# Kernel tuning notes

Measured on AMD Instinct MI355X. Metric: run time of the kernel, lower is better.

## Reference

```python
import jax, jax.numpy as jnp
import numpy as np
from jax import lax

EPS = 1e-5

def _bn(x):
    # BatchNorm1d, training-mode batch stats, affine at init (gamma=1, beta=0)
    return (x - x.mean(0)) / jnp.sqrt(x.var(0) + EPS)

def _nonlinear(x, W1, W2):
    h = jax.nn.relu(_bn(x @ W1.T))
    return jax.nn.relu(_bn(h @ W2.T))

def _conv_bn_lrelu(x, w):
    # x: [E, C, L], w: [O, C, 3], padding=1; BN over (batch, length)
    y = lax.conv_general_dilated(x, w, (1,), [(1, 1)], dimension_numbers=('NCH', 'OIH', 'NCH'))
    m = y.mean((0, 2), keepdims=True)
    v = y.var((0, 2), keepdims=True)
    y = (y - m) / jnp.sqrt(v + EPS)
    return jnp.where(y >= 0, y, 0.01 * y)  # LeakyReLU(negative_slope=0.01)

def _curve_encoder(x, c1, c2, c3, fc):
    y = _conv_bn_lrelu(x, c1)
    y = _conv_bn_lrelu(y, c2)
    y = _conv_bn_lrelu(y, c3)
    y = y.mean(-1)            # AdaptiveAvgPool1d(1)
    return _bn(y @ fc.T)      # _fc: Linear(bias=False) + BN, no activation

def _forward(attn_bias, angle, centroid_distance, edge_data, edge_type,
             edge_length, edge_convexity, node_feat,
             sd_emb, virt, angle_W1, angle_W2, cent_W1, cent_W2,
             etype_W1, etype_W2, elen_W1, elen_W2, econv_W1, econv_W2,
             curv_c1, curv_c2, curv_c3, curv_fc, edis_w,
             ec_Wp, ec_W1, ec_W2,
             shortest_distance, edge_path, edge_padding_mask, src, dst):
    B, N, _ = shortest_distance.shape
    H = sd_emb.shape[1]
    D = edge_path.shape[-1]           # multi_hop_max_dist
    n_edge = edge_padding_mask.shape[1]

    bias = jnp.broadcast_to(attn_bias[:, None], (B, H, N + 1, N + 1))

    # shortest-distance / angle / centroid biases, all [B, H, N, N]
    sdb = sd_emb[shortest_distance].transpose(0, 3, 1, 2)
    ang = _nonlinear(angle.reshape(-1, 1), angle_W1, angle_W2).reshape(B, N, N, H).transpose(0, 3, 1, 2)
    cen = _nonlinear(centroid_distance.reshape(-1, 1), cent_W1, cent_W2).reshape(B, N, N, H).transpose(0, 3, 1, 2)

    # --- multi_hop branch ---
    ef = (_curve_encoder(edge_data.transpose(0, 2, 1), curv_c1, curv_c2, curv_c3, curv_fc)
          + _nonlinear(edge_type, etype_W1, etype_W2)
          + _nonlinear(edge_length[:, None], elen_W1, elen_W2)
          + _nonlinear(edge_convexity, econv_W1, econv_W2))     # [E, H]
    # EdgeConv (UV-Net style node_cat): proj(n[src]) + proj(n[dst]) + efeat -> MLP -> BN -> ReLU
    proj = node_feat @ ec_Wp.T
    agg = proj[src] + proj[dst] + ef
    h = jax.nn.relu(_bn(agg @ ec_W1.T)) @ ec_W2.T
    ef2 = jax.nn.relu(_bn(h))                                   # [E, H]

    # edge_padding_mask is all-False, so edge_feature[edge_pos] = ef2 is a plain
    # row-major reshape; slot n_edge stays zero (padding target of edge_path)
    edge_feature = jnp.zeros((B, n_edge + 1, H), dtype=edge_data.dtype)
    edge_feature = edge_feature.at[:, :n_edge].set(ef2.reshape(B, n_edge, H))

    sd_ = jnp.where(shortest_distance == 0, 1, shortest_distance)
    sd_ = jnp.where(sd_ > 1, sd_ - 1, sd_)
    sd_ = jnp.clip(sd_, 0, D)

    ep = edge_path.reshape(B, N * N * D)
    eb = jnp.take_along_axis(edge_feature, ep[:, :, None], axis=1).reshape(B, N, N, D, H)
    Wd = edis_w.reshape(-1, H, H)[:D]                           # [D, H, H]
    eb = jnp.einsum('bijdh,dhk->bijk', eb, Wd)                  # per-hop bmm fused with hop-sum
    eb = eb / (sd_.astype(eb.dtype)[..., None] + 1e-6)
    eb = jnp.nan_to_num(eb)
    ebias = eb.transpose(0, 3, 1, 2)                            # [B, H, N, N]

    bias = bias.at[:, :, 1:, 1:].add(sdb + ang + cen + ebias)
    t = virt.reshape(1, H, 1)
    bias = bias.at[:, :, 1:, 0].add(t)
    bias = bias.at[:, :, 0, :].add(t)
    return bias + attn_bias[:, None]


def setup_inputs() -> dict:
    key = jax.random.key(0)
    ks = iter(jax.random.split(key, 48))
    B, N, H, D = 4, 256, 16, 5
    n_edge, n_pts = 1024, 20
    dim_node, num_distance, num_edge_dis = 256, 512, 128
    E = B * n_edge
    tot_nodes = B * N
    rn = lambda *s: jax.random.normal(next(ks), s, jnp.float32)
    return {
        'attn_bias': rn(B, N + 1, N + 1),
        'shortest_distance': jax.random.randint(next(ks), (B, N, N), 0, num_distance),
        'angle': rn(B, N, N),
        'centroid_distance': rn(B, N, N),
        'edge_path': jax.random.randint(next(ks), (B, N, N, D), 0, n_edge + 1),
        'edge_data': rn(E, n_pts, 12),
        'edge_type': rn(E, 11),
        'edge_length': rn(E),
        'edge_convexity': rn(E, 3),
        'edge_padding_mask': jnp.zeros((B, n_edge), dtype=bool),
        'src': jax.random.randint(next(ks), (E,), 0, tot_nodes),
        'dst': jax.random.randint(next(ks), (E,), 0, tot_nodes),
        'node_feat': rn(tot_nodes, dim_node),
        'sd_emb': (rn(num_distance, H) * 0.02).at[0].set(0.0),  # padding_idx=0
        'virt': rn(1, H) * 0.02,
        'angle_W1': rn(H, 1) * 0.1, 'angle_W2': rn(H, H) * 0.1,
        'cent_W1': rn(H, 1) * 0.1, 'cent_W2': rn(H, H) * 0.1,
        'etype_W1': rn(H, 11) * 0.1, 'etype_W2': rn(H, H) * 0.1,
        'elen_W1': rn(H, 1) * 0.1, 'elen_W2': rn(H, H) * 0.1,
        'econv_W1': rn(H, 3) * 0.1, 'econv_W2': rn(H, H) * 0.1,
        'curv_c1': rn(64, 12, 3) * 0.1, 'curv_c2': rn(128, 64, 3) * 0.05,
        'curv_c3': rn(256, 128, 3) * 0.05, 'curv_fc': rn(H, 256) * 0.05,
        'edis_w': rn(num_edge_dis * H * H, 1) * 0.02,
        'ec_Wp': rn(H, dim_node) * 0.02, 'ec_W1': rn(64, H) * 0.02, 'ec_W2': rn(H, 64) * 0.02,
    }


def reference(attn_bias, shortest_distance, angle, centroid_distance, edge_path,
              edge_data, edge_type, edge_length, edge_convexity, edge_padding_mask,
              src, dst, node_feat, sd_emb, virt, angle_W1, angle_W2, cent_W1, cent_W2,
              etype_W1, etype_W2, elen_W1, elen_W2, econv_W1, econv_W2,
              curv_c1, curv_c2, curv_c3, curv_fc, edis_w, ec_Wp, ec_W1, ec_W2):
    return _forward(attn_bias, angle, centroid_distance, edge_data, edge_type,
                    edge_length, edge_convexity, node_feat,
                    sd_emb, virt, angle_W1, angle_W2, cent_W1, cent_W2,
                    etype_W1, etype_W2, elen_W1, elen_W2, econv_W1, econv_W2,
                    curv_c1, curv_c2, curv_c3, curv_fc, edis_w,
                    ec_Wp, ec_W1, ec_W2,
                    shortest_distance, edge_path, edge_padding_mask, src, dst)
```

## Files before the change

### kernel.cpp

```cpp
#include <hip/hip_runtime.h>

#define EPSB 1e-5f
#define B_ 4
#define N_ 256
#define H_ 16
#define D_ 5
#define E_ 4096
#define M_PAIR (B_*N_*N_)

typedef __attribute__((ext_vector_type(8))) short short8;
typedef __attribute__((ext_vector_type(4))) float f32x4;

enum {
  SO_ANGX = 0,
  SO_CENX = 2,
  SO_MOMA = 16,
  SO_MOMC = 24,
  SO_FC   = 992, SO_FCQ   = 1008,
  SO_ET1  = 1024, SO_ET1Q = 1040,
  SO_ET2  = 1056, SO_ET2Q = 1072,
  SO_EL1  = 1088, SO_EL1Q = 1104,
  SO_EL2  = 1120, SO_EL2Q = 1136,
  SO_EV1  = 1152, SO_EV1Q = 1168,
  SO_EV2  = 1184, SO_EV2Q = 1200,
  SO_G1   = 1216, SO_G1Q  = 1280,
  SO_G2   = 1344, SO_G2Q  = 1360,
  SP_C1   = 2048,
  SP_C2   = SP_C1 + 32*512,
  SP_C3   = SP_C2 + 32*512,
  PSTATS_END = SP_C3 + 32*512
};

static constexpr size_t F_Y13  = 51200;
static constexpr size_t F_Y2   = F_Y13 + 10485760;
static constexpr size_t F_POOL = F_Y2 + 5242880;
static constexpr size_t F_FCB  = F_POOL + 1048576;
static constexpr size_t F_EF   = F_FCB + 65536;
static constexpr size_t F_PROJ = F_EF + 65536;
static constexpr size_t F_Z1EC = F_PROJ + 16384;
static constexpr size_t F_Z2T  = F_Z1EC + 262144;
static constexpr size_t F_G    = F_Z2T + 196608;
static constexpr size_t F_WT2  = F_G + 328000;
static constexpr size_t F_WT3  = F_WT2 + 12288;

__device__ __forceinline__ float waveSum(float v){
  #pragma unroll
  for(int o=32;o;o>>=1) v += __shfl_down(v,o);
  return v;
}

__device__ __forceinline__ ushort f2bf(float f){
  uint u = __float_as_uint(f);
  uint r = (u + 0x7FFF + ((u>>16)&1)) >> 16;
  return (ushort)r;
}
__device__ __forceinline__ float bf2f(ushort u){
  return __uint_as_float(((uint)u)<<16);
}

__device__ __forceinline__ void red32_atomic(float* ws, int so, int soq, float* s, float* q){
  __shared__ float red[4][32];
  int tid=threadIdx.x, lane=tid&63, wid=tid>>6;
  #pragma unroll
  for(int k=0;k<16;k++){
    float rs=waveSum(s[k]), rq=waveSum(q[k]);
    if(lane==0){ red[wid][k]=rs; red[wid][16+k]=rq; }
  }
  __syncthreads();
  if(tid<32){
    float t=red[0][tid]+red[1][tid]+red[2][tid]+red[3][tid];
    atomicAdd(&ws[tid<16 ? so+tid : soq+(tid-16)], t);
  }
}

__global__ __launch_bounds__(256) void k_conv1(const float* __restrict__ ed,
    const float* __restrict__ w, float* __restrict__ ws){
  __shared__ float wsh[64*37];
  __shared__ float xs[8*12*20];
  __shared__ float reds[256], redq[256];
  int tid=threadIdx.x;
  for(int i=tid;i<2304;i+=256){ int o=i/36, r=i%36; wsh[o*37+r]=w[i]; }
  int e0=blockIdx.x*8;
  for(int i=tid;i<1920;i+=256){
    int e=i/240, r=i%240, l=r/12, c=r%12;
    xs[(e*12+c)*20+l]=ed[(size_t)(e0+e)*240+r];
  }
  __syncthreads();
  int o=tid&63, eg=tid>>6;
  ushort* y1=(ushort*)(ws+F_Y13);
  float ssum=0, ssq=0;
  for(int ee=0;ee<2;ee++){
    int e=eg*2+ee;
    float acc[20];
    #pragma unroll
    for(int l=0;l<20;l++) acc[l]=0;
    for(int c=0;c<12;c++){
      float w0=wsh[o*37+c*3], w1=wsh[o*37+c*3+1], w2=wsh[o*37+c*3+2];
      const float* xr=xs+(e*12+c)*20;
      #pragma unroll
      for(int l=0;l<20;l++){
        acc[l]=fmaf(w1,xr[l],acc[l]);
        if(l>0)  acc[l]=fmaf(w0,xr[l-1],acc[l]);
        if(l<19) acc[l]=fmaf(w2,xr[l+1],acc[l]);
      }
    }
    size_t base=((size_t)(e0+e)*20)*64;
    #pragma unroll
    for(int l=0;l<20;l++){
      y1[base+(size_t)l*64+o]=f2bf(acc[l]);
      ssum+=acc[l]; ssq+=acc[l]*acc[l];
    }
  }
  reds[eg*64+o]=ssum; redq[eg*64+o]=ssq;
  __syncthreads();
  int g=blockIdx.x&31;
  if(tid<64){
    atomicAdd(&ws[SP_C1+g*512+tid], reds[tid]+reds[64+tid]+reds[128+tid]+reds[192+tid]);
  } else if(tid<128){
    int oo=tid-64;
    atomicAdd(&ws[SP_C1+g*512+256+oo], redq[oo]+redq[64+oo]+redq[128+oo]+redq[192+oo]);
  }
}


__device__ void dev_wprep(int bid, const float* __restrict__ c2w,
    const float* __restrict__ c3w, ushort* __restrict__ wt2, ushort* __restrict__ wt3){
  int t = bid*256 + threadIdx.x;
  if(t < 128*192){
    int idx=t;
    int j=idx&7, lane=(idx>>3)&63, ks=(idx>>9)%6, ct=idx/3072;
    int l16=lane&15, lhi=lane>>4;
    int o=ct*16+l16, tap=ks/2, c=(ks%2)*32+lhi*8+j;
    wt2[idx]=f2bf(c2w[(o*64+c)*3+tap]);
  } else {
    int idx=t-128*192;
    if(idx<256*384){
      int j=idx&7, lane=(idx>>3)&63, ks=(idx>>9)%12, ct=idx/6144;
      int l16=lane&15, lhi=lane>>4;
      int o=ct*16+l16, tap=ks/4, c=(ks%4)*32+lhi*8+j;
      wt3[idx]=f2bf(c3w[(o*128+c)*3+tap]);
    }
  }
}

__device__ void dev_proj(int bid, const float* __restrict__ nf,
    const float* __restrict__ Wp, float* __restrict__ ws, char* pool){
  float* wps=(float*)pool;
  int tid=threadIdx.x;
  for(int i=tid;i<4096;i+=256){ wps[(i>>8)*260+(i&255)]=Wp[i]; }
  __syncthreads();
  int t=bid*256+tid;
  int v=t>>4, h=t&15;
  const float4* row=(const float4*)(nf+(size_t)v*256);
  const float4* wr=(const float4*)(wps+h*260);
  float z=0;
  #pragma unroll 8
  for(int c=0;c<64;c++){
    float4 a=row[c], b=wr[c];
    z+=a.x*b.x+a.y*b.y+a.z*b.z+a.w*b.w;
  }
  ws[F_PROJ+t]=z;
}

__device__ void dev_scalar(int bid, const float* __restrict__ ang,
    const float* __restrict__ cen, float* __restrict__ st){
  int tid = bid*256 + threadIdx.x;
  float sa=0, qa=0, sc=0, qc=0;
  for(int i=tid; i<M_PAIR; i += 256*256){
    float a=ang[i], c=cen[i];
    sa+=a; qa+=a*a; sc+=c; qc+=c*c;
  }
  __shared__ float red[4][4];
  int lane=threadIdx.x&63, wid=threadIdx.x>>6;
  sa=waveSum(sa); qa=waveSum(qa); sc=waveSum(sc); qc=waveSum(qc);
  if(lane==0){ red[wid][0]=sa; red[wid][1]=qa; red[wid][2]=sc; red[wid][3]=qc; }
  __syncthreads();
  if(threadIdx.x<4){
    float t=red[0][threadIdx.x]+red[1][threadIdx.x]+red[2][threadIdx.x]+red[3][threadIdx.x];
    atomicAdd(&st[threadIdx.x], t);
  }
}

template<int DIM>
__device__ void dev_sml1(const float* __restrict__ x,
    const float* __restrict__ W1, float* __restrict__ ws, int so, int soq, int bid){
  __shared__ float w1s[176];
  int tid=threadIdx.x;
  if(tid<16*DIM) w1s[tid]=W1[tid];
  __syncthreads();
  int e=bid*256+tid;
  float xv[DIM];
  #pragma unroll
  for(int j=0;j<DIM;j++) xv[j]=x[(size_t)e*DIM+j];
  float s[16], q[16];
  #pragma unroll
  for(int k=0;k<16;k++){
    float z=0;
    #pragma unroll
    for(int j=0;j<DIM;j++) z+=w1s[k*DIM+j]*xv[j];
    s[k]=z; q[k]=z*z;
  }
  red32_atomic(ws, so, soq, s, q);
}

__global__ __launch_bounds__(256) void k_misc(
    const float* __restrict__ c2w, const float* __restrict__ c3w,
    const float* __restrict__ nf, const float* __restrict__ Wp,
    const float* __restrict__ ang, const float* __restrict__ cen,
    const float* __restrict__ et, const float* __restrict__ el, const float* __restrict__ ev,
    const float* __restrict__ etW1, const float* __restrict__ elW1, const float* __restrict__ evW1,
    float* __restrict__ ws){
  __shared__ char pool[16640];
  int bx=blockIdx.x;
  if(bx<480)       dev_wprep(bx, c2w, c3w, (ushort*)(ws+F_WT2), (ushort*)(ws+F_WT3));
  else if(bx<544)  dev_proj(bx-480, nf, Wp, ws, pool);
  else if(bx<800)  dev_scalar(bx-544, ang, cen, ws);
  else {
    int bid=bx-800;
    int g=bid>>4, b2=bid&15;
    if(g==0)      dev_sml1<11>(et,etW1,ws,SO_ET1,SO_ET1Q,b2);
    else if(g==1) dev_sml1<1> (el,elW1,ws,SO_EL1,SO_EL1Q,b2);
    else          dev_sml1<3> (ev,evW1,ws,SO_EV1,SO_EV1Q,b2);
  }
}


__device__ void dev_mom2(int bid, const float* __restrict__ x, float* __restrict__ st,
    int soX, int mo){
  int tid=threadIdx.x;
  float mu = st[soX]*(1.0f/262144.0f);
  float P=0,N=0,Pq=0,Nq=0;
  for(int i=bid*256+tid; i<M_PAIR; i+=32*256){
    float dx=x[i]-mu;
    if(dx>0){ P+=dx; Pq+=dx*dx; } else { N+=dx; Nq+=dx*dx; }
  }
  __shared__ float red[4][4];
  int lane=tid&63, wid=tid>>6;
  P=waveSum(P); N=waveSum(N); Pq=waveSum(Pq); Nq=waveSum(Nq);
  if(lane==0){ red[wid][0]=P; red[wid][1]=N; red[wid][2]=Pq; red[wid][3]=Nq; }
  __syncthreads();
  if(tid<4){
    float t=red[0][tid]+red[1][tid]+red[2][tid]+red[3][tid];
    atomicAdd(&st[mo+tid], t);
  }
}

template<int DIM>
__device__ void dev_sml2(const float* __restrict__ x,
    const float* __restrict__ W1, const float* __restrict__ W2,
    float* __restrict__ ws, int so1, int so1q, int so2, int so2q,
    float* __restrict__ z2out, int bid){
  __shared__ float w1s[176];
  __shared__ float w2s[256];
  __shared__ float mi[16][2];
  int tid=threadIdx.x;
  if(tid<16*DIM) w1s[tid]=W1[tid];
  w2s[tid]=W2[tid];
  if(tid<16){
    float m=ws[so1+tid]*(1.0f/4096.0f);
    float v=ws[so1q+tid]*(1.0f/4096.0f)-m*m; if(v<0)v=0;
    mi[tid][0]=m; mi[tid][1]=rsqrtf(v+EPSB);
  }
  __syncthreads();
  int e=bid*256+tid;
  float xv[DIM];
  #pragma unroll
  for(int j=0;j<DIM;j++) xv[j]=x[(size_t)e*DIM+j];
  float h1[16];
  #pragma unroll
  for(int h=0;h<16;h++){
    float z=0;
    #pragma unroll
    for(int j=0;j<DIM;j++) z+=w1s[h*DIM+j]*xv[j];
    z=(z-mi[h][0])*mi[h][1];
    h1[h]=z>0?z:0;
  }
  float s[16], q[16];
  #pragma unroll
  for(int k=0;k<16;k++){
    float z=0;
    #pragma unroll
    for(int h=0;h<16;h++) z+=w2s[k*16+h]*h1[h];
    z2out[(size_t)e*16+k]=z;
    s[k]=z; q[k]=z*z;
  }
  red32_atomic(ws, so2, so2q, s, q);
}

__global__ __launch_bounds__(256) void k_stats2(
    const float* __restrict__ ang, const float* __restrict__ cen,
    const float* __restrict__ et, const float* __restrict__ el, const float* __restrict__ ev,
    const float* __restrict__ etW1, const float* __restrict__ etW2,
    const float* __restrict__ elW1, const float* __restrict__ elW2,
    const float* __restrict__ evW1, const float* __restrict__ evW2,
    float* __restrict__ ws){
  int bx=blockIdx.x;
  if(bx<32)       dev_mom2(bx, ang, ws, SO_ANGX, SO_MOMA);
  else if(bx<64)  dev_mom2(bx-32, cen, ws, SO_CENX, SO_MOMC);
  else {
    int bid=bx-64;
    int g=bid>>4, b2=bid&15;
    if(g==0)      dev_sml2<11>(et,etW1,etW2,ws,SO_ET1,SO_ET1Q,SO_ET2,SO_ET2Q,ws+F_Z2T,b2);
    else if(g==1) dev_sml2<1> (el,elW1,elW2,ws,SO_EL1,SO_EL1Q,SO_EL2,SO_EL2Q,ws+F_Z2T+65536,b2);
    else          dev_sml2<3> (ev,evW1,evW2,ws,SO_EV1,SO_EV1Q,SO_EV2,SO_EV2Q,ws+F_Z2T+131072,b2);
  }
}

template<int CIN, int OUT, int EPB, int NSPLIT>
__global__ __launch_bounds__(256) void k_convmf(
    const ushort* __restrict__ yin, const ushort* __restrict__ wt,
    ushort* __restrict__ yout, float* __restrict__ ws,
    int spIn, int spOut)
{
  constexpr int K = CIN*3;
  constexpr int KSTEPS = K/32;
  constexpr int M = EPB*20;
  constexpr int ROWT = M/16;
  constexpr int WCOLT = OUT/(64*NSPLIT);
  constexpr int ROWS = EPB*22;
  constexpr int RB = CIN*2;
  constexpr uint SWZ = RB/16 - 1;
  __shared__ ushort xs[ROWS*CIN];
  __shared__ float mi[CIN][2];
  int tid = threadIdx.x;
  int bx = blockIdx.x;
  int eblk = bx / NSPLIT, split = bx % NSPLIT;
  int lane = tid&63, wid = tid>>6;
  int l16 = lane&15, lhi = lane>>4;
  int colbase = (split*4 + wid) * (OUT/(4*NSPLIT));

  short8 bF[WCOLT][KSTEPS];
  #pragma unroll
  for(int n=0;n<WCOLT;n++){
    const ushort* wp = wt + ((size_t)(colbase/16 + n)*KSTEPS)*512 + (size_t)lane*8;
    #pragma unroll
    for(int ks=0;ks<KSTEPS;ks++) bF[n][ks]=*(const short8*)(wp + (size_t)ks*512);
  }

  for(int c=tid; c<CIN; c+=256){
    float s=0,q=0;
    #pragma unroll
    for(int g=0;g<32;g++){ s+=ws[spIn+g*512+c]; q+=ws[spIn+g*512+256+c]; }
    float m=s*(1.0f/81920.0f);
    float v=q*(1.0f/81920.0f)-m*m; if(v<0)v=0;
    mi[c][0]=m; mi[c][1]=rsqrtf(v+EPSB);
  }
  uint* xs32 = (uint*)xs;
  for(int i=tid; i<EPB*2*(CIN/2); i+=256){
    int e=i/(CIN), r=i%(CIN); int lp = (r < CIN/2)? 0:21; int cw = r%(CIN/2);
    xs32[(e*22+lp)*(CIN/2)+cw]=0;
  }
  __syncthreads();
  int e0 = eblk*EPB;
  const ushort* src = yin + (size_t)e0*20*CIN;
  for(int i=tid; i<EPB*20*(CIN/8); i+=256){
    int c8 = i%(CIN/8); int rl = i/(CIN/8);
    int c = c8*8;
    short8 v = *(const short8*)(src + (size_t)rl*CIN + c);
    uint pk[4];
    #pragma unroll
    for(int jj=0;jj<4;jj++){
      float f0 = bf2f((ushort)v[jj*2]);
      float f1 = bf2f((ushort)v[jj*2+1]);
      f0=(f0-mi[c+jj*2  ][0])*mi[c+jj*2  ][1]; f0= f0>=0?f0:0.01f*f0;
      f1=(f1-mi[c+jj*2+1][0])*mi[c+jj*2+1][1]; f1= f1>=0?f1:0.01f*f1;
      pk[jj] = (uint)f2bf(f0) | ((uint)f2bf(f1)<<16);
    }
    int e = rl/20, l=rl%20;
    int row = e*22 + l + 1;
    uint byteoff = (uint)row*RB + (((uint)c*2) ^ (uint)((row&SWZ)<<4));
    *(uint4*)((char*)xs + byteoff) = make_uint4(pk[0],pk[1],pk[2],pk[3]);
  }
  __syncthreads();

  f32x4 acc[ROWT][WCOLT];
  #pragma unroll
  for(int m=0;m<ROWT;m++)
    #pragma unroll
    for(int n=0;n<WCOLT;n++) acc[m][n]=(f32x4){0,0,0,0};
  int rowc[ROWT];
  #pragma unroll
  for(int m=0;m<ROWT;m++){ int r=m*16+l16; rowc[m]=(r/20)*22 + (r%20); }

  short8 aF0[ROWT], aF1[ROWT];

#define LOADA(ksv, A) { \
    int t_=(ksv)/(CIN/32); int c0_=((ksv)%(CIN/32))*32 + lhi*8; \
    _Pragma("unroll") \
    for(int m=0;m<ROWT;m++){ \
      int row_=rowc[m]+t_; \
      uint off_=(uint)row_*RB + (((uint)c0_*2) ^ (uint)((row_&SWZ)<<4)); \
      A[m]=*(const short8*)((char*)xs+off_); } }

#define MFMAK(A, ksv) { \
    _Pragma("unroll") \
    for(int m=0;m<ROWT;m++) \
      _Pragma("unroll") \
      for(int n=0;n<WCOLT;n++) \
        acc[m][n]=__builtin_amdgcn_mfma_f32_16x16x32_bf16(A[m],bF[n][ksv],acc[m][n],0,0,0); }

  LOADA(0, aF0);
  #pragma unroll
  for(int kp=0; kp<KSTEPS/2; kp++){
    LOADA(kp*2+1, aF1);
    MFMAK(aF0, kp*2);
    if(kp*2+2<KSTEPS) LOADA(kp*2+2, aF0);
    MFMAK(aF1, kp*2+1);
  }
#undef LOADA
#undef MFMAK

  int g=bx&31;
  #pragma unroll
  for(int n=0;n<WCOLT;n++){
    float s=0,q=0;
    #pragma unroll
    for(int m=0;m<ROWT;m++)
      #pragma unroll
      for(int j=0;j<4;j++){ float a=acc[m][n][j]; s+=a; q+=a*a; }
    s += __shfl_xor(s,16); s += __shfl_xor(s,32);
    q += __shfl_xor(q,16); q += __shfl_xor(q,32);
    if(lhi==0){
      int o = colbase+n*16+l16;
      atomicAdd(&ws[spOut+g*512+o], s);
      atomicAdd(&ws[spOut+g*512+256+o], q);
    }
  }
  ushort* dst = yout + (size_t)eblk*M*OUT;
  #pragma unroll
  for(int m=0;m<ROWT;m++)
    #pragma unroll
    for(int j=0;j<4;j++){
      int R = m*16 + lhi*4 + j;
      #pragma unroll
      for(int n=0;n<WCOLT;n++)
        dst[(size_t)R*OUT + colbase + n*16 + l16] = f2bf(acc[m][n][j]);
    }
}

__global__ __launch_bounds__(256) void k_poolfc(const float* __restrict__ fcw, float* __restrict__ ws){
  __shared__ float ps[16][260];
  __shared__ float red[4][32];
  __shared__ float mo[256][2];
  int tid=threadIdx.x;
  {
    float s=0,q=0;
    #pragma unroll
    for(int g=0;g<32;g++){ s+=ws[SP_C3+g*512+tid]; q+=ws[SP_C3+g*512+256+tid]; }
    float m=s*(1.0f/81920.0f);
    float v=q*(1.0f/81920.0f)-m*m; if(v<0)v=0;
    mo[tid][0]=m; mo[tid][1]=rsqrtf(v+EPSB);
  }
  __syncthreads();
  int e0=blockIdx.x*16;
  const ushort* y3=(const ushort*)(ws+F_Y13);
  float m=mo[tid][0], inv=mo[tid][1];
  for(int el=0;el<16;el++){
    const ushort* row=y3+((size_t)(e0+el)*20)*256+tid;
    float s=0;
    #pragma unroll
    for(int l=0;l<20;l++){
      float x=(bf2f(row[(size_t)l*256])-m)*inv;
      s += x>=0.f? x : 0.01f*x;
    }
    ps[el][tid]=s*(1.0f/20.0f);
  }
  __syncthreads();
  int e=tid>>4, h=tid&15;
  const float* wr=fcw+(size_t)h*256;
  float z=0;
  for(int c=0;c<256;c++) z+=ps[e][c]*wr[c];
  ws[F_FCB+(size_t)(e0+e)*16+h]=z;
  float s=z, q=z*z;
  #pragma unroll
  for(int o=16;o<64;o<<=1){ s+=__shfl_down(s,o); q+=__shfl_down(q,o); }
  int lane=tid&63, wid=tid>>6;
  if(lane<16){ red[wid][lane]=s; red[wid][16+lane]=q; }
  __syncthreads();
  if(tid<32){
    float v=red[0][tid]+red[1][tid]+red[2][tid]+red[3][tid];
    atomicAdd(&ws[tid<16? SO_FC+tid : SO_FCQ+(tid-16)], v);
  }
}

__device__ __constant__ int EF_BASES[4][2] = {
  {SO_ET2,SO_ET2Q},{SO_EL2,SO_EL2Q},{SO_EV2,SO_EV2Q},{SO_FC,SO_FCQ}
};

__global__ __launch_bounds__(256) void k_aggef(const int* __restrict__ src, const int* __restrict__ dst,
    const float* __restrict__ ecW1, float* __restrict__ ws){
  __shared__ float w1s[64*17];
  __shared__ float mi[4][16][2];
  __shared__ float aLDS[32][17];
  __shared__ float zLDS[64][33];
  __shared__ float reds[4][64], redq[4][64];
  int tid=threadIdx.x;
  for(int i=tid;i<1024;i+=256) w1s[(i>>4)*17+(i&15)]=ecW1[i];
  if(tid<64){
    int g=tid>>4, h=tid&15;
    float m=ws[EF_BASES[g][0]+h]*(1.0f/4096.0f);
    float v=ws[EF_BASES[g][1]+h]*(1.0f/4096.0f)-m*m; if(v<0)v=0;
    mi[g][h][0]=m; mi[g][h][1]=rsqrtf(v+EPSB);
  }
  __syncthreads();
  int e0=blockIdx.x*32;
  for(int it=tid; it<32*16; it+=256){
    int el=it>>4, h=it&15;
    int e=e0+el;
    float z=ws[F_FCB+(size_t)e*16+h];
    float a=(z-mi[3][h][0])*mi[3][h][1];
    #pragma unroll
    for(int g=0;g<3;g++){
      float z2=ws[F_Z2T+(size_t)g*65536+(size_t)e*16+h];
      float r=(z2-mi[g][h][0])*mi[g][h][1];
      a+= r>0?r:0;
    }
    int s=src[e], d=dst[e];
    a+=ws[F_PROJ+(size_t)s*16+h]+ws[F_PROJ+(size_t)d*16+h];
    aLDS[el][h]=a;
  }
  __syncthreads();
  int o=tid&63, elq=tid>>6;
  float s=0,q=0;
  #pragma unroll
  for(int j=0;j<8;j++){
    int el=elq*8+j;
    float z=0;
    #pragma unroll
    for(int h=0;h<16;h++) z+=w1s[o*17+h]*aLDS[el][h];
    zLDS[o][el]=z;
    s+=z; q+=z*z;
  }
  reds[elq][o]=s; redq[elq][o]=q;
  __syncthreads();
  for(int idx=tid; idx<2048; idx+=256){
    int oo=idx>>5, el=idx&31;
    ws[F_Z1EC+(size_t)oo*E_+e0+el]=zLDS[oo][el];
  }
  if(tid<64){
    atomicAdd(&ws[SO_G1+tid], reds[0][tid]+reds[1][tid]+reds[2][tid]+reds[3][tid]);
  } else if(tid<128){
    int oo=tid-64;
    atomicAdd(&ws[SO_G1Q+oo], redq[0][oo]+redq[1][oo]+redq[2][oo]+redq[3][oo]);
  }
}

__global__ __launch_bounds__(256) void k_ec2(const float* __restrict__ ecW2, float* __restrict__ ws){
  __shared__ float w2s[1024];
  __shared__ float mi[64][2];
  int tid=threadIdx.x;
  for(int i=tid;i<1024;i+=256) w2s[i]=ecW2[i];
  if(tid<64){
    float m=ws[SO_G1+tid]*(1.0f/4096.0f);
    float v=ws[SO_G1Q+tid]*(1.0f/4096.0f)-m*m; if(v<0)v=0;
    mi[tid][0]=m; mi[tid][1]=rsqrtf(v+EPSB);
  }
  __syncthreads();
  int el=tid&63, kq=tid>>6;
  int e=blockIdx.x*64+el;
  float acc[4]={0,0,0,0};
  #pragma unroll 8
  for(int o=0;o<64;o++){
    float z=ws[F_Z1EC+(size_t)o*E_+e];
    float h=(z-mi[o][0])*mi[o][1];
    h=h>0?h:0;
    #pragma unroll
    for(int j=0;j<4;j++) acc[j]+=w2s[(kq*4+j)*64+o]*h;
  }
  #pragma unroll
  for(int j=0;j<4;j++) ws[F_FCB+(size_t)e*16+kq*4+j]=acc[j];
  #pragma unroll
  for(int j=0;j<4;j++){
    float rs=waveSum(acc[j]);
    float rq=waveSum(acc[j]*acc[j]);
    if(el==0){
      atomicAdd(&ws[SO_G2+kq*4+j], rs);
      atomicAdd(&ws[SO_G2Q+kq*4+j], rq);
    }
  }
}

__global__ __launch_bounds__(256) void k_ef2g(const float* __restrict__ edisw, float* __restrict__ ws){
  __shared__ float wd[1280];
  __shared__ float mi[16][2];
  int tid=threadIdx.x;
  for(int i=tid;i<1280;i+=256) wd[i]=edisw[i];
  if(tid<16){
    float m=ws[SO_G2+tid]*(1.0f/4096.0f);
    float va=ws[SO_G2Q+tid]*(1.0f/4096.0f)-m*m; if(va<0)va=0;
    mi[tid][0]=m; mi[tid][1]=rsqrtf(va+EPSB);
  }
  __syncthreads();
  int t=blockIdx.x*256+tid;
  if(t>=4*1025*5) return;
  int bp=t/5, d=t%5;
  int b=bp/1025, pos=bp%1025;
  float ef[16];
  if(pos<1024){
    int e=b*1024+pos;
    #pragma unroll
    for(int k=0;k<16;k++){
      float z=ws[F_FCB+(size_t)e*16+k];
      float v=(z-mi[k][0])*mi[k][1];
      ef[k]= v>0?v:0;
    }
  } else {
    #pragma unroll
    for(int k=0;k<16;k++) ef[k]=0;
  }
  float* g=ws+F_G+(size_t)bp*80+d*16;
  const float* wdd=wd+d*256;
  #pragma unroll
  for(int k=0;k<16;k++){
    float s=0;
    #pragma unroll
    for(int h=0;h<16;h++) s+=ef[h]*wdd[h*16+k];
    g[k]=s;
  }
}

__global__ __launch_bounds__(256) void k_pair(const float* __restrict__ ab,
    const int* __restrict__ sd, const float* __restrict__ ang, const float* __restrict__ cen,
    const int* __restrict__ ep, const float* __restrict__ sdemb,
    const float* __restrict__ angW1, const float* __restrict__ angW2,
    const float* __restrict__ cenW1, const float* __restrict__ cenW2,
    const float* __restrict__ ws, float* __restrict__ out){
  __shared__ float cpa[16],cma[16],m2a[16],i2a[16];
  __shared__ float cpc[16],cmc[16],m2c[16],i2c[16];
  __shared__ float mv[4];
  int tid=threadIdx.x;
  if(tid==0){
    float s=ws[SO_ANGX], q=ws[SO_ANGX+1];
    float mu=s*(1.0f/262144.0f);
    float v=q*(1.0f/262144.0f)-mu*mu; if(v<0)v=0;
    mv[0]=mu; mv[1]=v;
    s=ws[SO_CENX]; q=ws[SO_CENX+1];
    mu=s*(1.0f/262144.0f);
    v=q*(1.0f/262144.0f)-mu*mu; if(v<0)v=0;
    mv[2]=mu; mv[3]=v;
  }
  __syncthreads();
  if(tid<32){
    int k=tid&15; bool isC = tid>=16;
    const float* W1=isC?cenW1:angW1; const float* W2=isC?cenW2:angW2;
    float var=isC?mv[3]:mv[1];
    float cp=0, cm=0;
    for(int h=0;h<16;h++){
      float w=W1[h];
      float A=w*rsqrtf(var*w*w+EPSB);
      float wk=W2[k*16+h];
      if(A>0) cp+=wk*A; else cm+=wk*A;
    }
    int mo = isC? SO_MOMC : SO_MOMA;
    float P=ws[mo], N=ws[mo+1], Pq=ws[mo+2], Nq=ws[mo+3];
    float mean=(cp*P+cm*N)*(1.0f/262144.0f);
    float e2=(cp*cp*Pq+cm*cm*Nq)*(1.0f/262144.0f);
    float v2=e2-mean*mean; if(v2<0)v2=0;
    float iv=rsqrtf(v2+EPSB);
    if(!isC){ cpa[k]=cp; cma[k]=cm; m2a[k]=mean; i2a[k]=iv; }
    else    { cpc[k]=cp; cmc[k]=cm; m2c[k]=mean; i2c[k]=iv; }
  }
  __syncthreads();
  int t=blockIdx.x*256+tid;
  int b=t>>16, rem=t&65535, i=rem>>8, j=rem&255;
  int sdv=sd[t];
  float xa=ang[t], xc0=cen[t];
  float acc[16];
  const float* se=sdemb+(size_t)sdv*16;
  #pragma unroll
  for(int k=0;k<16;k++) acc[k]=se[k];
  {
    float dx=xa-mv[0];
    bool pos=dx>0.f;
    #pragma unroll
    for(int k=0;k<16;k++){
      float z=dx*(pos?cpa[k]:cma[k]);
      float r=(z-m2a[k])*i2a[k];
      acc[k]+= r>0?r:0;
    }
  }
  {
    float dx=xc0-mv[2];
    bool pos=dx>0.f;
    #pragma unroll
    for(int k=0;k<16;k++){
      float z=dx*(pos?cpc[k]:cmc[k]);
      float r=(z-m2c[k])*i2c[k];
      acc[k]+= r>0?r:0;
    }
  }
  {
    int sdm = sdv==0 ? 1 : sdv;
    if(sdm>1) sdm-=1;
    if(sdm>5) sdm=5;
    float inv=1.0f/((float)sdm+1e-6f);
    float eb[16];
    #pragma unroll
    for(int k=0;k<16;k++) eb[k]=0;
    const float* G=ws+F_G;
    #pragma unroll
    for(int d=0;d<5;d++){
      int idx=ep[(size_t)t*5+d];
      const float4* g=(const float4*)(G+(size_t)(b*1025+idx)*80+d*16);
      float4 g0=g[0], g1=g[1], g2=g[2], g3=g[3];
      eb[0]+=g0.x; eb[1]+=g0.y; eb[2]+=g0.z; eb[3]+=g0.w;
      eb[4]+=g1.x; eb[5]+=g1.y; eb[6]+=g1.z; eb[7]+=g1.w;
      eb[8]+=g2.x; eb[9]+=g2.y; eb[10]+=g2.z; eb[11]+=g2.w;
      eb[12]+=g3.x; eb[13]+=g3.y; eb[14]+=g3.z; eb[15]+=g3.w;
    }
    #pragma unroll
    for(int k=0;k<16;k++) acc[k]+=eb[k]*inv;
  }
  float base2=2.0f*ab[(size_t)b*66049+(size_t)(i+1)*257+(j+1)];
  #pragma unroll
  for(int k=0;k<16;k++)
    out[(((size_t)b*16+k)*257+(i+1))*257+(j+1)]=acc[k]+base2;
}

__global__ __launch_bounds__(256) void k_border(const float* __restrict__ ab,
    const float* __restrict__ virt, float* __restrict__ out){
  int t=blockIdx.x*256+threadIdx.x;
  if(t>=4*16*513) return;
  int idx=t%513, bh=t/513;
  int b=bh>>4, h=bh&15;
  float v=virt[h];
  if(idx<257){
    out[(((size_t)b*16+h)*257)*257+idx]=2.0f*ab[(size_t)b*66049+idx]+v;
  } else {
    int p=idx-256;
    out[(((size_t)b*16+h)*257+p)*257]=2.0f*ab[(size_t)b*66049+(size_t)p*257]+v;
  }
}

extern "C" void kernel_launch(void* const* d_in, const int* in_sizes, int n_in,
                              void* d_out, int out_size, void* d_ws, size_t ws_size,
                              hipStream_t stream) {
  const float* ab    =(const float*)d_in[0];
  const int*   sdist =(const int*)  d_in[1];
  const float* ang   =(const float*)d_in[2];
  const float* cen   =(const float*)d_in[3];
  const int*   ep    =(const int*)  d_in[4];
  const float* edata =(const float*)d_in[5];
  const float* etype =(const float*)d_in[6];
  const float* elen  =(const float*)d_in[7];
  const float* econv =(const float*)d_in[8];
  const int*   src   =(const int*)  d_in[10];
  const int*   dst   =(const int*)  d_in[11];
  const float* nf    =(const float*)d_in[12];
  const float* sdemb =(const float*)d_in[13];
  const float* virt  =(const float*)d_in[14];
  const float* angW1 =(const float*)d_in[15];
  const float* angW2 =(const float*)d_in[16];
  const float* cenW1 =(const float*)d_in[17];
  const float* cenW2 =(const float*)d_in[18];
  const float* etW1  =(const float*)d_in[19];
  const float* etW2  =(const float*)d_in[20];
  const float* elW1  =(const float*)d_in[21];
  const float* elW2  =(const float*)d_in[22];
  const float* evW1  =(const float*)d_in[23];
  const float* evW2  =(const float*)d_in[24];
  const float* c1w   =(const float*)d_in[25];
  const float* c2w   =(const float*)d_in[26];
  const float* c3w   =(const float*)d_in[27];
  const float* fcw   =(const float*)d_in[28];
  const float* edisw =(const float*)d_in[29];
  const float* ecWp  =(const float*)d_in[30];
  const float* ecW1  =(const float*)d_in[31];
  const float* ecW2  =(const float*)d_in[32];
  float* ws=(float*)d_ws;
  float* out=(float*)d_out;

  hipMemsetAsync(d_ws, 0, PSTATS_END*sizeof(float), stream);

  k_conv1<<<512,256,0,stream>>>(edata,c1w,ws);
  k_misc<<<848,256,0,stream>>>(c2w,c3w,nf,ecWp,ang,cen,
                               etype,elen,econv,etW1,elW1,evW1,ws);
  k_stats2<<<112,256,0,stream>>>(ang,cen,etype,elen,econv,
                                 etW1,etW2,elW1,elW2,evW1,evW2,ws);

  k_convmf<64,128,4,2><<<2048,256,0,stream>>>((const ushort*)(ws+F_Y13),(const ushort*)(ws+F_WT2),
                                              (ushort*)(ws+F_Y2),ws,SP_C1,SP_C2);
  k_convmf<128,256,4,2><<<2048,256,0,stream>>>((const ushort*)(ws+F_Y2),(const ushort*)(ws+F_WT3),
                                               (ushort*)(ws+F_Y13),ws,SP_C2,SP_C3);
  k_poolfc<<<256,256,0,stream>>>(fcw,ws);

  k_aggef<<<128,256,0,stream>>>(src,dst,ecW1,ws);
  k_ec2<<<64,256,0,stream>>>(ecW2,ws);
  k_ef2g<<<81,256,0,stream>>>(edisw,ws);

  k_pair<<<1024,256,0,stream>>>(ab,sdist,ang,cen,ep,sdemb,angW1,angW2,cenW1,cenW2,ws,out);
  k_border<<<129,256,0,stream>>>(ab,virt,out);
}
```

Baseline: 185.8 us.

## Stream conv weights per k-step and stage output through LDS for coalesced stores

The conv MFMA kernel no longer preloads every weight fragment into registers. It now double-buffers the B fragments per k-step alongside the A loads, which cuts register pressure and may raise occupancy. The output tile is first written into padded shared memory, reusing the input buffer, then copied to global memory as 16-byte row-contiguous stores instead of scattered 2-byte stores. In exchange, weight loads from global memory now sit inside the MFMA loop, and there are two extra barriers plus possibly more LDS use.

```diff
diff --git a/kernel.cpp b/kernel.cpp
--- a/kernel.cpp
+++ b/kernel.cpp
@@ -317,25 +317,26 @@
   constexpr int M = EPB*20;
   constexpr int ROWT = M/16;
   constexpr int WCOLT = OUT/(64*NSPLIT);
+  constexpr int COLS = OUT/NSPLIT;
+  constexpr int OST = COLS + 8;
   constexpr int ROWS = EPB*22;
   constexpr int RB = CIN*2;
   constexpr uint SWZ = RB/16 - 1;
-  __shared__ ushort xs[ROWS*CIN];
+  constexpr int XS_ELEMS = (ROWS*CIN > M*OST) ? ROWS*CIN : M*OST;
+  __shared__ ushort xs[XS_ELEMS];
   __shared__ float mi[CIN][2];
   int tid = threadIdx.x;
   int bx = blockIdx.x;
   int eblk = bx / NSPLIT, split = bx % NSPLIT;
   int lane = tid&63, wid = tid>>6;
   int l16 = lane&15, lhi = lane>>4;
-  int colbase = (split*4 + wid) * (OUT/(4*NSPLIT));
-
-  short8 bF[WCOLT][KSTEPS];
-  #pragma unroll
-  for(int n=0;n<WCOLT;n++){
-    const ushort* wp = wt + ((size_t)(colbase/16 + n)*KSTEPS)*512 + (size_t)lane*8;
-    #pragma unroll
-    for(int ks=0;ks<KSTEPS;ks++) bF[n][ks]=*(const short8*)(wp + (size_t)ks*512);
-  }
+  int colbase = (split*4 + wid) * (COLS/4);
+  int lcolbase = wid * (COLS/4);
+
+  const ushort* wp[WCOLT];
+  #pragma unroll
+  for(int n=0;n<WCOLT;n++)
+    wp[n] = wt + ((size_t)(colbase/16 + n)*KSTEPS)*512 + (size_t)lane*8;
 
   for(int c=tid; c<CIN; c+=256){
     float s=0,q=0;
@@ -382,7 +383,7 @@
   #pragma unroll
   for(int m=0;m<ROWT;m++){ int r=m*16+l16; rowc[m]=(r/20)*22 + (r%20); }
 
-  short8 aF0[ROWT], aF1[ROWT];
+  short8 aF0[ROWT], aF1[ROWT], b0[WCOLT], b1[WCOLT];
 
 #define LOADA(ksv, A) { \
     int t_=(ksv)/(CIN/32); int c0_=((ksv)%(CIN/32))*32 + lhi*8; \
@@ -392,22 +393,27 @@
       uint off_=(uint)row_*RB + (((uint)c0_*2) ^ (uint)((row_&SWZ)<<4)); \
       A[m]=*(const short8*)((char*)xs+off_); } }
 
-#define MFMAK(A, ksv) { \
+#define LOADB(ksv, Bv) { \
+    _Pragma("unroll") \
+    for(int n=0;n<WCOLT;n++) Bv[n]=*(const short8*)(wp[n] + (size_t)(ksv)*512); }
+
+#define MFMAK(A, Bv) { \
     _Pragma("unroll") \
     for(int m=0;m<ROWT;m++) \
       _Pragma("unroll") \
       for(int n=0;n<WCOLT;n++) \
-        acc[m][n]=__builtin_amdgcn_mfma_f32_16x16x32_bf16(A[m],bF[n][ksv],acc[m][n],0,0,0); }
-
-  LOADA(0, aF0);
+        acc[m][n]=__builtin_amdgcn_mfma_f32_16x16x32_bf16(A[m],Bv[n],acc[m][n],0,0,0); }
+
+  LOADA(0, aF0); LOADB(0, b0);
   #pragma unroll
   for(int kp=0; kp<KSTEPS/2; kp++){
-    LOADA(kp*2+1, aF1);
-    MFMAK(aF0, kp*2);
-    if(kp*2+2<KSTEPS) LOADA(kp*2+2, aF0);
-    MFMAK(aF1, kp*2+1);
+    LOADA(kp*2+1, aF1); LOADB(kp*2+1, b1);
+    MFMAK(aF0, b0);
+    if(kp*2+2<KSTEPS){ LOADA(kp*2+2, aF0); LOADB(kp*2+2, b0); }
+    MFMAK(aF1, b1);
   }
 #undef LOADA
+#undef LOADB
 #undef MFMAK
 
   int g=bx&31;
@@ -426,7 +432,8 @@
       atomicAdd(&ws[spOut+g*512+256+o], q);
     }
   }
-  ushort* dst = yout + (size_t)eblk*M*OUT;
+
+  __syncthreads();
   #pragma unroll
   for(int m=0;m<ROWT;m++)
     #pragma unroll
@@ -434,8 +441,15 @@
       int R = m*16 + lhi*4 + j;
       #pragma unroll
       for(int n=0;n<WCOLT;n++)
-        dst[(size_t)R*OUT + colbase + n*16 + l16] = f2bf(acc[m][n][j]);
-    }
+        xs[(size_t)R*OST + lcolbase + n*16 + l16] = f2bf(acc[m][n][j]);
+    }
+  __syncthreads();
+  ushort* dst = yout + (size_t)eblk*M*OUT + (size_t)split*COLS;
+  for(int idx=tid; idx<M*(COLS/8); idx+=256){
+    int row = idx/(COLS/8), c8 = idx%(COLS/8);
+    uint4 v = *(const uint4*)&xs[(size_t)row*OST + c8*8];
+    *(uint4*)&dst[(size_t)row*OUT + c8*8] = v;
+  }
 }
 
 __global__ __launch_bounds__(256) void k_poolfc(const float* __restrict__ fcw, float* __restrict__ ws){
```

After: 177.6 us. 1.05x faster.
